# Optimization experiments

Measured on AMD Instinct MI355X. Metric: run time of the kernel, lower is better.

## Reference

```python
import jax, jax.numpy as jnp
import numpy as np

B, S, D = 32, 512, 768
M, T = 32, 30
H, DFF, L, E = 12, 3072, 4, 100000
HD = D // H


def _layer_norm(x, w, b):
    m = jnp.mean(x, axis=-1, keepdims=True)
    v = jnp.var(x, axis=-1, keepdims=True)
    return (x - m) * jax.lax.rsqrt(v + 1e-5) * w + b


def _encoder_layer(x, p):
    # torch.nn.TransformerEncoderLayer, batch_first, post-LN, relu, eval (no dropout)
    wi, bi, wo, bo, g1, b1, w1, c1, w2, c2, g2, b2 = p
    qkv = x @ wi.T + bi                                   # [B,M,3D]
    q, k, v = jnp.split(qkv, 3, axis=-1)
    q = q.reshape(B, M, H, HD)
    k = k.reshape(B, M, H, HD)
    v = v.reshape(B, M, H, HD)
    a = jnp.einsum('bqhd,bkhd->bhqk', q, k) / np.float32(np.sqrt(HD))
    a = jax.nn.softmax(a, axis=-1)
    o = jnp.einsum('bhqk,bkhd->bqhd', a, v).reshape(B, M, D)
    x = _layer_norm(x + o @ wo.T + bo, g1, b1)
    ff = jax.nn.relu(x @ w1.T + c1) @ w2.T + c2
    return _layer_norm(x + ff, g2, b2)


def _forward(lhs, attn_w, attn_b, Wi, Bi, Wo, Bo, G1, B1, W1, C1, W2, C2, G2, B2v,
             cls_w1, cls_w2, cls_b2, pos, emask):
    # Vectorized form of the source triple loop: token slot x of mention (i,j) is
    # copied from last_hidden_state[i, x] while no -1 has been seen (break) and
    # the mention is active (entity_attention_mask != 0).
    valid = jnp.cumprod((pos != -1).astype(jnp.int32), axis=-1) > 0      # [B,M,T]
    valid = valid & (emask[:, :, None] != 0)
    mentions = jnp.where(valid[..., None], lhs[:, None, :T, :], 0.0)     # [B,M,T,D]
    scores = jax.nn.softmax(jnp.einsum('bmtd,d->bmt', mentions, attn_w) + attn_b, axis=-1)
    x = jnp.einsum('bmt,bmtd->bmd', scores, mentions)                    # attention pool
    for l in range(L):
        x = _encoder_layer(x, (Wi[l], Bi[l], Wo[l], Bo[l], G1[l], B1[l],
                               W1[l], C1[l], W2[l], C2[l], G2[l], B2v[l]))
    return (x @ cls_w1.T) @ cls_w2.T + cls_b2                            # [B,M,E]


def setup_inputs() -> dict:
    key = jax.random.key(0)
    k = jax.random.split(key, 12)
    lhs = jax.random.normal(k[0], (B, S, D), jnp.float32)
    pos = jax.random.randint(k[1], (B, M, T), 0, S)
    lens = jax.random.randint(k[2], (B, M), 0, T + 1)
    pos = jnp.where(jnp.arange(T)[None, None, :] < lens[..., None], pos, -1)
    emask = jax.random.randint(k[3], (B, M), 0, 2)
    s = 0.02
    return {
        'last_hidden_state': lhs,
        'attn_w': jax.random.normal(k[4], (D,), jnp.float32) * s,
        'attn_b': jnp.zeros((), jnp.float32),
        'in_proj_w': jax.random.normal(k[5], (L, 3 * D, D), jnp.float32) * s,
        'in_proj_b': jnp.zeros((L, 3 * D), jnp.float32),
        'out_w': jax.random.normal(k[6], (L, D, D), jnp.float32) * s,
        'out_b': jnp.zeros((L, D), jnp.float32),
        'ln1_w': jnp.ones((L, D), jnp.float32),
        'ln1_b': jnp.zeros((L, D), jnp.float32),
        'lin1_w': jax.random.normal(k[7], (L, DFF, D), jnp.float32) * s,
        'lin1_b': jnp.zeros((L, DFF), jnp.float32),
        'lin2_w': jax.random.normal(k[8], (L, D, DFF), jnp.float32) * s,
        'lin2_b': jnp.zeros((L, D), jnp.float32),
        'ln2_w': jnp.ones((L, D), jnp.float32),
        'ln2_b': jnp.zeros((L, D), jnp.float32),
        'cls_w1': jax.random.normal(k[9], (100, D), jnp.float32) * s,
        'cls_w2': jax.random.normal(k[10], (E, 100), jnp.float32) * s,
        'cls_b2': jnp.zeros((E,), jnp.float32),
        'entity_position_ids': pos,
        'entity_attention_mask': emask,
    }


def reference(last_hidden_state, attn_w, attn_b, in_proj_w, in_proj_b, out_w, out_b,
              ln1_w, ln1_b, lin1_w, lin1_b, lin2_w, lin2_b, ln2_w, ln2_b,
              cls_w1, cls_w2, cls_b2, entity_position_ids, entity_attention_mask):
    return _forward(last_hidden_state, attn_w, attn_b, in_proj_w, in_proj_b, out_w, out_b,
                    ln1_w, ln1_b, lin1_w, lin1_b, lin2_w, lin2_b, ln2_w, ln2_b,
                    cls_w1, cls_w2, cls_b2, entity_position_ids, entity_attention_mask)
```

## Files before the change

### kernel.cpp

```cpp
#include <hip/hip_runtime.h>

constexpr int Bc = 32, Sc = 512, Dc = 768, Mc = 32, Tc = 30;
constexpr int Hc = 12, DFFc = 3072, Lc = 4, Ec = 100000, HDc = 64;
constexpr int TOK = Bc * Mc;
constexpr int KC2 = 128;

typedef float floatx4 __attribute__((ext_vector_type(4)));
typedef __bf16 bfrag8 __attribute__((ext_vector_type(8)));
typedef unsigned short usx8 __attribute__((ext_vector_type(8)));
typedef unsigned short usx4 __attribute__((ext_vector_type(4)));

__device__ __forceinline__ unsigned short f32_to_bf16(float f) {
    unsigned int u = __float_as_uint(f);
    unsigned int r = (u + 0x7FFFu + ((u >> 16) & 1u)) >> 16;
    return (unsigned short)r;
}

__device__ __forceinline__ void gload_lds16(const void* gsrc, void* lds) {
    __builtin_amdgcn_global_load_lds((const unsigned int*)gsrc, (unsigned int*)lds, 16, 0, 0);
}

struct CvtSegs {
    const float* src[7];
    unsigned short* dst[7];
    unsigned int end[7];
    unsigned int total;
};

constexpr int FB_CVT1 = 1536, FB_CVT2 = 512, FB_POOL = TOK;

__global__ __launch_bounds__(256)
void front_kernel(CvtSegs a, const float* __restrict__ cw2, unsigned short* __restrict__ bw_c2,
                  const float* __restrict__ lhs, const float* __restrict__ attn_w,
                  const int* __restrict__ pos, const int* __restrict__ emask,
                  float* __restrict__ x0, unsigned short* __restrict__ x0b) {
    const int bid = blockIdx.x;
    const int tid = threadIdx.x;

    if (bid < FB_CVT1) {
        const unsigned int stride = FB_CVT1 * 256;
        for (unsigned int i = bid * 256 + tid; i < a.total; i += stride) {
            int s = 0;
            while (i >= a.end[s]) ++s;
            const unsigned int off = i - (s ? a.end[s - 1] : 0u);
            usx4 o = (usx4)0;
            if (a.src[s]) {
                floatx4 v = *(const floatx4*)(a.src[s] + 4 * (size_t)off);
                #pragma unroll
                for (int j = 0; j < 4; ++j) o[j] = f32_to_bf16(v[j]);
            }
            *(usx4*)(a.dst[s] + 4 * (size_t)off) = o;
        }
        return;
    }
    if (bid < FB_CVT1 + FB_CVT2) {
        const int total = Ec * (KC2 / 8);
        const int stride = FB_CVT2 * 256;
        for (int c = (bid - FB_CVT1) * 256 + tid; c < total; c += stride) {
            const int row = c >> 4, j = c & 15;
            const int col0 = j * 8;
            const float* sp = cw2 + (size_t)row * 100 + col0;
            usx8 o = (usx8)0;
            if (col0 + 8 <= 100) {
                floatx4 v0 = *(const floatx4*)(sp);
                floatx4 v1 = *(const floatx4*)(sp + 4);
                #pragma unroll
                for (int jj = 0; jj < 4; ++jj) { o[jj] = f32_to_bf16(v0[jj]); o[4 + jj] = f32_to_bf16(v1[jj]); }
            } else if (col0 < 100) {
                #pragma unroll
                for (int jj = 0; jj < 8; ++jj)
                    if (col0 + jj < 100) o[jj] = f32_to_bf16(sp[jj]);
            }
            *(usx8*)(bw_c2 + (size_t)row * KC2 + col0) = o;
        }
        return;
    }

    const int bm = bid - (FB_CVT1 + FB_CVT2);
    const int b = bm >> 5;
    __shared__ float s_logit[32];
    __shared__ float s_w[32];
    __shared__ int s_valid[32];

    if (tid == 0) {
        int em = emask[bm];
        int ok = 1;
        for (int t = 0; t < Tc; ++t) {
            if (pos[bm * Tc + t] == -1) ok = 0;
            s_valid[t] = (ok && em) ? 1 : 0;
        }
    }
    __syncthreads();

    const int wid = tid >> 6, lane = tid & 63;
    for (int t = wid; t < Tc; t += 4) {
        float p = 0.f;
        const float* row = lhs + ((size_t)b * Sc + t) * Dc;
        for (int d = lane; d < Dc; d += 64) p += row[d] * attn_w[d];
        #pragma unroll
        for (int off = 32; off > 0; off >>= 1) p += __shfl_down(p, off);
        if (lane == 0) s_logit[t] = s_valid[t] ? p : 0.0f;
    }
    __syncthreads();
    if (tid == 0) {
        float mx = -1e30f;
        for (int t = 0; t < Tc; ++t) mx = fmaxf(mx, s_logit[t]);
        float sum = 0.f;
        for (int t = 0; t < Tc; ++t) { float e = expf(s_logit[t] - mx); s_w[t] = e; sum += e; }
        float inv = 1.0f / sum;
        for (int t = 0; t < Tc; ++t) s_w[t] = s_valid[t] ? s_w[t] * inv : 0.0f;
    }
    __syncthreads();
    for (int d = tid; d < Dc; d += 256) {
        float acc = 0.f;
        for (int t = 0; t < Tc; ++t) acc += s_w[t] * lhs[((size_t)b * Sc + t) * Dc + d];
        x0[(size_t)bm * Dc + d] = acc;
        x0b[(size_t)bm * Dc + d] = f32_to_bf16(acc);
    }
}

template <int BM, int BN, int WM, int WN, int OUTBF>
__global__ __launch_bounds__(256)
void gemm_bf16_kernel(const unsigned short* __restrict__ A, int lda,
                      const unsigned short* __restrict__ B, int ldb,
                      const float* __restrict__ bias, void* __restrict__ Cv,
                      int ldc, int M, int N, int K, int relu, int nxReal) {
    constexpr int BK = 64;
    __shared__ unsigned short lA[2][BM * BK];
    __shared__ unsigned short lB[2][BN * BK];

    int bx, by;
    if (nxReal > 0) {
        const int gx = gridDim.x, gy = gridDim.y;
        const int lb = blockIdx.y * gx + blockIdx.x;
        const int xcd = lb & 7, p = lb >> 3;
        const int pq = p / gy;
        bx = xcd * (gx >> 3) + pq;
        by = p - pq * gy;
        if (bx >= nxReal) return;
    } else {
        bx = blockIdx.x; by = blockIdx.y;
    }
    const int z = blockIdx.z;
    A += (size_t)z * K;
    B += (size_t)z * K;

    const int tid = threadIdx.x;
    const int bm0 = by * BM;
    const int bn0 = bx * BN;

    const int wid = tid >> 6;
    const int lane = tid & 63;
    const int quad = lane >> 4;
    const int l16 = lane & 15;
    const int wr = (wid >> 1) * (WM * 16);
    const int wc = (wid & 1) * (WN * 16);

    floatx4 acc[WM][WN] = {};

    auto stageA = [&](int buf, int k0) {
        #pragma unroll
        for (int it = 0; it < BM / 32; ++it) {
            const int chunk = wid * (BM / 32) + it;
            const int boff = chunk * 1024 + lane * 16;
            const int row = boff >> 7;
            const int cb = (boff & 127) ^ ((row & 7) << 4);
            gload_lds16((const char*)(A + (size_t)(bm0 + row) * lda + k0) + cb,
                        &lA[buf][chunk * 512]);
        }
    };
    auto stageB = [&](int buf, int k0) {
        #pragma unroll
        for (int it = 0; it < BN / 32; ++it) {
            const int chunk = wid * (BN / 32) + it;
            const int boff = chunk * 1024 + lane * 16;
            const int row = boff >> 7;
            const int cb = (boff & 127) ^ ((row & 7) << 4);
            gload_lds16((const char*)(B + (size_t)(bn0 + row) * ldb + k0) + cb,
                        &lB[buf][chunk * 512]);
        }
    };

    stageA(0, 0);
    stageB(0, 0);
    __syncthreads();

    int c = 0;
    for (int k0 = 0; k0 < K; k0 += BK, c ^= 1) {
        const int kn = k0 + BK;
        const bool more = (kn < K);
        if (more) { stageA(c ^ 1, kn); stageB(c ^ 1, kn); }
        const unsigned short* bA = lA[c];
        const unsigned short* bB = lB[c];
        #pragma unroll
        for (int kk = 0; kk < BK; kk += 32) {
            bfrag8 af[WM], bfr[WN];
            #pragma unroll
            for (int i = 0; i < WM; ++i) {
                const int rowA = wr + i * 16 + l16;
                af[i] = *(const bfrag8*)((const char*)bA + rowA * 128 +
                                         ((kk * 2 + quad * 16) ^ ((rowA & 7) << 4)));
            }
            #pragma unroll
            for (int j = 0; j < WN; ++j) {
                const int rowB = wc + j * 16 + l16;
                bfr[j] = *(const bfrag8*)((const char*)bB + rowB * 128 +
                                          ((kk * 2 + quad * 16) ^ ((rowB & 7) << 4)));
            }
            #pragma unroll
            for (int i = 0; i < WM; ++i)
                #pragma unroll
                for (int j = 0; j < WN; ++j)
                    acc[i][j] = __builtin_amdgcn_mfma_f32_16x16x32_bf16(af[i], bfr[j], acc[i][j], 0, 0, 0);
        }
        if (more) __syncthreads();
    }

    #pragma unroll
    for (int i = 0; i < WM; ++i) {
        #pragma unroll
        for (int j = 0; j < WN; ++j) {
            const int col = bn0 + wc + j * 16 + l16;
            if (col < N) {
                const int row0 = bm0 + wr + i * 16 + quad * 4;
                const float bv = bias ? bias[col] : 0.0f;
                #pragma unroll
                for (int r = 0; r < 4; ++r) {
                    float v = acc[i][j][r] + bv;
                    if (relu) v = fmaxf(v, 0.0f);
                    const size_t idx = (size_t)z * M * ldc + (size_t)(row0 + r) * ldc + col;
                    if (OUTBF) ((unsigned short*)Cv)[idx] = f32_to_bf16(v);
                    else       ((float*)Cv)[idx] = v;
                }
            }
        }
    }
}

__global__ __launch_bounds__(256)
void attn_kernel(const float* __restrict__ qkv, unsigned short* __restrict__ outb) {
    const int bh = blockIdx.x;
    const int b = bh / Hc, h = bh % Hc;
    const int tid = threadIdx.x;
    __shared__ float sQ[32][65];
    __shared__ float sK[32][65];
    __shared__ float sV[32][65];
    __shared__ float sS[32][33];

    const int m = tid >> 3;
    const int c0 = (tid & 7) * 8;
    {
        const size_t rbase = ((size_t)(b * 32 + m)) * (3 * Dc);
        #pragma unroll
        for (int j = 0; j < 8; ++j) {
            sQ[m][c0 + j] = qkv[rbase + h * HDc + c0 + j];
            sK[m][c0 + j] = qkv[rbase + Dc + h * HDc + c0 + j];
            sV[m][c0 + j] = qkv[rbase + 2 * Dc + h * HDc + c0 + j];
        }
    }
    __syncthreads();

    #pragma unroll
    for (int u = 0; u < 4; ++u) {
        const int e = tid * 4 + u;
        const int q = e >> 5, k = e & 31;
        float s = 0.f;
        #pragma unroll
        for (int d = 0; d < HDc; ++d) s += sQ[q][d] * sK[k][d];
        sS[q][k] = s * 0.125f;
    }
    __syncthreads();
    if (tid < 32) {
        float mx = -1e30f;
        for (int k = 0; k < 32; ++k) mx = fmaxf(mx, sS[tid][k]);
        float sum = 0.f;
        for (int k = 0; k < 32; ++k) { float e = expf(sS[tid][k] - mx); sS[tid][k] = e; sum += e; }
        const float inv = 1.0f / sum;
        for (int k = 0; k < 32; ++k) sS[tid][k] *= inv;
    }
    __syncthreads();
    float o[8] = {};
    for (int k = 0; k < 32; ++k) {
        const float p = sS[m][k];
        #pragma unroll
        for (int j = 0; j < 8; ++j) o[j] += p * sV[k][c0 + j];
    }
    usx8 o8;
    #pragma unroll
    for (int j = 0; j < 8; ++j) o8[j] = f32_to_bf16(o[j]);
    *(usx8*)(&outb[((size_t)(b * 32 + m)) * Dc + h * HDc + c0]) = o8;
}

__global__ __launch_bounds__(256)
void addln_kernel(const float* __restrict__ xa, const float* __restrict__ xs, int nslab,
                  const float* __restrict__ badd, const float* __restrict__ g,
                  const float* __restrict__ be, float* __restrict__ outf,
                  unsigned short* __restrict__ outb) {
    const int row = blockIdx.x;
    const int tid = threadIdx.x;
    __shared__ float red[8];
    float v[3];
    float s = 0.f, sq = 0.f;
    #pragma unroll
    for (int i = 0; i < 3; ++i) {
        const int d = tid + i * 256;
        float x = xa[(size_t)row * Dc + d] + badd[d];
        for (int sl = 0; sl < nslab; ++sl)
            x += xs[((size_t)sl * TOK + row) * Dc + d];
        v[i] = x; s += x; sq += x * x;
    }
    #pragma unroll
    for (int off = 32; off > 0; off >>= 1) {
        s += __shfl_down(s, off);
        sq += __shfl_down(sq, off);
    }
    if ((tid & 63) == 0) { red[tid >> 6] = s; red[4 + (tid >> 6)] = sq; }
    __syncthreads();
    const float ts = red[0] + red[1] + red[2] + red[3];
    const float tq = red[4] + red[5] + red[6] + red[7];
    const float mean = ts * (1.0f / Dc);
    const float var = tq * (1.0f / Dc) - mean * mean;
    const float inv = rsqrtf(var + 1e-5f);
    #pragma unroll
    for (int i = 0; i < 3; ++i) {
        const int d = tid + i * 256;
        const float y = (v[i] - mean) * inv * g[d] + be[d];
        outf[(size_t)row * Dc + d] = y;
        outb[(size_t)row * Dc + d] = f32_to_bf16(y);
    }
}

extern "C" void kernel_launch(void* const* d_in, const int* in_sizes, int n_in,
                              void* d_out, int out_size, void* d_ws, size_t ws_size,
                              hipStream_t stream) {
    const float* lhs   = (const float*)d_in[0];
    const float* attnw = (const float*)d_in[1];
    const float* ipw = (const float*)d_in[3];
    const float* ipb = (const float*)d_in[4];
    const float* oww = (const float*)d_in[5];
    const float* owb = (const float*)d_in[6];
    const float* g1  = (const float*)d_in[7];
    const float* b1  = (const float*)d_in[8];
    const float* l1w = (const float*)d_in[9];
    const float* l1b = (const float*)d_in[10];
    const float* l2w = (const float*)d_in[11];
    const float* l2b = (const float*)d_in[12];
    const float* g2  = (const float*)d_in[13];
    const float* b2  = (const float*)d_in[14];
    const float* cw1 = (const float*)d_in[15];
    const float* cw2 = (const float*)d_in[16];
    const float* cb2 = (const float*)d_in[17];
    const int* pos   = (const int*)d_in[18];
    const int* emask = (const int*)d_in[19];
    float* out = (float*)d_out;

    constexpr size_t N_IP = (size_t)Lc * 3 * Dc * Dc;
    constexpr size_t N_OW = (size_t)Lc * Dc * Dc;
    constexpr size_t N_L1 = (size_t)Lc * DFFc * Dc;
    constexpr size_t N_L2 = (size_t)Lc * Dc * DFFc;
    constexpr size_t N_C1 = (size_t)KC2 * Dc;

    char* ws = (char*)d_ws;
    unsigned short* bw_c2 = (unsigned short*)ws;
    unsigned short* bufCb = bw_c2 + (size_t)Ec * KC2;

    constexpr size_t F_XA   = (size_t)TOK * Dc;
    constexpr size_t F_QKV  = (size_t)TOK * 3 * Dc;
    constexpr size_t F_SLAB = (size_t)4 * TOK * Dc;
    constexpr size_t S_ACT  = (size_t)TOK * Dc;
    constexpr size_t S_FFH  = (size_t)TOK * DFFc;
    constexpr size_t tail_bytes =
        4 * (F_XA + F_XA + F_QKV + F_SLAB) +
        2 * (N_IP + N_OW + N_L1 + N_L2 + N_C1 + 3 * S_ACT + S_FFH);

    const size_t out_bytes = (size_t)out_size * 4;
    char* tail = (char*)d_out + ((out_bytes - tail_bytes) & ~(size_t)255);

    float* xA   = (float*)tail;
    float* xB   = xA + F_XA;
    float* qkvb = xB + F_XA;
    float* bufS = qkvb + F_QKV;
    unsigned short* bw_ip = (unsigned short*)(bufS + F_SLAB);
    unsigned short* bw_ow = bw_ip + N_IP;
    unsigned short* bw_l1 = bw_ow + N_OW;
    unsigned short* bw_l2 = bw_l1 + N_L1;
    unsigned short* bw_c1 = bw_l2 + N_L2;
    unsigned short* xAb   = bw_c1 + N_C1;
    unsigned short* xBb   = xAb + S_ACT;
    unsigned short* attnb = xBb + S_ACT;
    unsigned short* bufHb = attnb + S_ACT;

    {
        CvtSegs segs{};
        const float* srcs[6] = {ipw, oww, l1w, l2w, cw1, nullptr};
        unsigned short* dsts[6] = {bw_ip, bw_ow, bw_l1, bw_l2, bw_c1, bw_c1 + (size_t)100 * Dc};
        const unsigned int cnt[6] = {(unsigned)(N_IP / 4), (unsigned)(N_OW / 4),
                                     (unsigned)(N_L1 / 4), (unsigned)(N_L2 / 4),
                                     (unsigned)(100 * Dc / 4), (unsigned)(28 * Dc / 4)};
        unsigned int acc = 0;
        for (int i = 0; i < 6; ++i) { segs.src[i] = srcs[i]; segs.dst[i] = dsts[i]; acc += cnt[i]; segs.end[i] = acc; }
        segs.src[6] = nullptr; segs.dst[6] = dsts[5]; segs.end[6] = 0xFFFFFFFFu;
        segs.total = acc;
        front_kernel<<<FB_CVT1 + FB_CVT2 + FB_POOL, 256, 0, stream>>>(
            segs, cw2, bw_c2, lhs, attnw, pos, emask, xA, xAb);
    }

    auto g64 = [&](const unsigned short* A, int lda, const unsigned short* B, int ldb,
                   const float* bias, void* C, int ldc, int N, int K, int relu,
                   int ks, int outbf, bool swz) {
        int gx = (N + 63) / 64, nx = -1;
        if (swz) { nx = gx; gx = (gx + 7) & ~7; }
        dim3 grid(gx, TOK / 64, ks);
        if (outbf) gemm_bf16_kernel<64, 64, 2, 2, 1><<<grid, 256, 0, stream>>>(A, lda, B, ldb, bias, C, ldc, TOK, N, K, relu, nx);
        else       gemm_bf16_kernel<64, 64, 2, 2, 0><<<grid, 256, 0, stream>>>(A, lda, B, ldb, bias, C, ldc, TOK, N, K, relu, nx);
    };

    for (int l = 0; l < Lc; ++l) {
        g64(xAb, Dc, bw_ip + (size_t)l * 3 * Dc * Dc, Dc, ipb + (size_t)l * 3 * Dc,
            qkvb, 3 * Dc, 3 * Dc, Dc, 0, 1, 0, false);
        attn_kernel<<<Bc * Hc, 256, 0, stream>>>(qkvb, attnb);
        g64(attnb, Dc, bw_ow + (size_t)l * Dc * Dc, Dc, nullptr,
            bufS, Dc, Dc, Dc / 4, 0, 4, 0, false);
        addln_kernel<<<TOK, 256, 0, stream>>>(xA, bufS, 4, owb + (size_t)l * Dc,
                                              g1 + (size_t)l * Dc, b1 + (size_t)l * Dc, xB, xBb);
        g64(xBb, Dc, bw_l1 + (size_t)l * DFFc * Dc, Dc, l1b + (size_t)l * DFFc,
            bufHb, DFFc, DFFc, Dc, 1, 1, 1, true);
        g64(bufHb, DFFc, bw_l2 + (size_t)l * Dc * DFFc, DFFc, nullptr,
            bufS, Dc, Dc, DFFc / 4, 0, 4, 0, false);
        addln_kernel<<<TOK, 256, 0, stream>>>(xB, bufS, 4, l2b + (size_t)l * Dc,
                                              g2 + (size_t)l * Dc, b2 + (size_t)l * Dc, xA, xAb);
    }

    g64(xAb, Dc, bw_c1, Dc, nullptr, bufCb, KC2, KC2, Dc, 0, 1, 1, false);
    {
        int nx = (Ec + 127) / 128;
        int gx = (nx + 7) & ~7;
        dim3 grid(gx, TOK / 128, 1);
        gemm_bf16_kernel<128, 128, 4, 4, 0><<<grid, 256, 0, stream>>>(
            bufCb, KC2, bw_c2, KC2, cb2, out, Ec, TOK, Ec, KC2, 0, nx);
    }
}
```

Baseline: 1.023 ms.

## Fuse QKV projection into attention kernel and drop GEMM double buffering

Replaces the separate QKV GEMM and attention kernel with one kernel per (batch, head). Each block computes its 32x192 Q/K/V slice with MFMA, keeps it in shared memory, and runs softmax attention there, so the fp32 QKV buffer never goes to global memory and one launch per layer disappears. The generic GEMM also moves from double-buffered LDS staging to a single buffer with a sync before and after compute. That cuts LDS use and may raise occupancy, but load latency is no longer overlapped with MFMA work in every GEMM, including the large classifier GEMM.

```diff
diff --git a/kernel.cpp b/kernel.cpp
--- a/kernel.cpp
+++ b/kernel.cpp
@@ -126,8 +126,8 @@
                       const float* __restrict__ bias, void* __restrict__ Cv,
                       int ldc, int M, int N, int K, int relu, int nxReal) {
     constexpr int BK = 64;
-    __shared__ unsigned short lA[2][BM * BK];
-    __shared__ unsigned short lB[2][BN * BK];
+    __shared__ unsigned short lA[BM * BK];
+    __shared__ unsigned short lB[BN * BK];
 
     int bx, by;
     if (nxReal > 0) {
@@ -158,7 +158,7 @@
 
     floatx4 acc[WM][WN] = {};
 
-    auto stageA = [&](int buf, int k0) {
+    for (int k0 = 0; k0 < K; k0 += BK) {
         #pragma unroll
         for (int it = 0; it < BM / 32; ++it) {
             const int chunk = wid * (BM / 32) + it;
@@ -166,10 +166,8 @@
             const int row = boff >> 7;
             const int cb = (boff & 127) ^ ((row & 7) << 4);
             gload_lds16((const char*)(A + (size_t)(bm0 + row) * lda + k0) + cb,
-                        &lA[buf][chunk * 512]);
-        }
-    };
-    auto stageB = [&](int buf, int k0) {
+                        &lA[chunk * 512]);
+        }
         #pragma unroll
         for (int it = 0; it < BN / 32; ++it) {
             const int chunk = wid * (BN / 32) + it;
@@ -177,34 +175,22 @@
             const int row = boff >> 7;
             const int cb = (boff & 127) ^ ((row & 7) << 4);
             gload_lds16((const char*)(B + (size_t)(bn0 + row) * ldb + k0) + cb,
-                        &lB[buf][chunk * 512]);
-        }
-    };
-
-    stageA(0, 0);
-    stageB(0, 0);
-    __syncthreads();
-
-    int c = 0;
-    for (int k0 = 0; k0 < K; k0 += BK, c ^= 1) {
-        const int kn = k0 + BK;
-        const bool more = (kn < K);
-        if (more) { stageA(c ^ 1, kn); stageB(c ^ 1, kn); }
-        const unsigned short* bA = lA[c];
-        const unsigned short* bB = lB[c];
+                        &lB[chunk * 512]);
+        }
+        __syncthreads();
         #pragma unroll
         for (int kk = 0; kk < BK; kk += 32) {
             bfrag8 af[WM], bfr[WN];
             #pragma unroll
             for (int i = 0; i < WM; ++i) {
                 const int rowA = wr + i * 16 + l16;
-                af[i] = *(const bfrag8*)((const char*)bA + rowA * 128 +
+                af[i] = *(const bfrag8*)((const char*)lA + rowA * 128 +
                                          ((kk * 2 + quad * 16) ^ ((rowA & 7) << 4)));
             }
             #pragma unroll
             for (int j = 0; j < WN; ++j) {
                 const int rowB = wc + j * 16 + l16;
-                bfr[j] = *(const bfrag8*)((const char*)bB + rowB * 128 +
+                bfr[j] = *(const bfrag8*)((const char*)lB + rowB * 128 +
                                           ((kk * 2 + quad * 16) ^ ((rowB & 7) << 4)));
             }
             #pragma unroll
@@ -213,7 +199,7 @@
                 for (int j = 0; j < WN; ++j)
                     acc[i][j] = __builtin_amdgcn_mfma_f32_16x16x32_bf16(af[i], bfr[j], acc[i][j], 0, 0, 0);
         }
-        if (more) __syncthreads();
+        __syncthreads();
     }
 
     #pragma unroll
@@ -238,35 +224,94 @@
 }
 
 __global__ __launch_bounds__(256)
-void attn_kernel(const float* __restrict__ qkv, unsigned short* __restrict__ outb) {
+void fqa_kernel(const unsigned short* __restrict__ xAb,
+                const unsigned short* __restrict__ bw_ip_l,
+                const float* __restrict__ ipb_l,
+                unsigned short* __restrict__ attnb) {
+    __shared__ __align__(16) char smem[29696];
+    unsigned short* sA = (unsigned short*)smem;
+    unsigned short* sB = (unsigned short*)(smem + 4096);
+    float* qkvf = (float*)smem;
+    float (*sS)[33] = (float(*)[33])(smem + 25344);
+
     const int bh = blockIdx.x;
-    const int b = bh / Hc, h = bh % Hc;
+    const int b32 = (bh / Hc) * 32;
+    const int h = bh % Hc;
     const int tid = threadIdx.x;
-    __shared__ float sQ[32][65];
-    __shared__ float sK[32][65];
-    __shared__ float sV[32][65];
-    __shared__ float sS[32][33];
+    const int wid = tid >> 6, lane = tid & 63;
+    const int quad = lane >> 4, l16 = lane & 15;
+
+    floatx4 acc[2][3] = {};
+
+    for (int k0 = 0; k0 < Dc; k0 += 64) {
+        #pragma unroll
+        for (int it = 0; it < 7; ++it) {
+            const int c = wid * 7 + it;
+            if (c < 4) {
+                const int boff = c * 1024 + lane * 16;
+                const int row = boff >> 7;
+                const int cb = (boff & 127) ^ ((row & 7) << 4);
+                gload_lds16((const char*)(xAb + (size_t)(b32 + row) * Dc + k0) + cb,
+                            &sA[c * 512]);
+            } else {
+                const int boff = (c - 4) * 1024 + lane * 16;
+                const int row = boff >> 7;
+                const int cb = (boff & 127) ^ ((row & 7) << 4);
+                const int grow = (row >> 6) * Dc + h * 64 + (row & 63);
+                gload_lds16((const char*)(bw_ip_l + (size_t)grow * Dc + k0) + cb,
+                            &sB[(c - 4) * 512]);
+            }
+        }
+        __syncthreads();
+        #pragma unroll
+        for (int kk = 0; kk < 64; kk += 32) {
+            bfrag8 af[2], bfr[3];
+            #pragma unroll
+            for (int i = 0; i < 2; ++i) {
+                const int rowA = i * 16 + l16;
+                af[i] = *(const bfrag8*)((const char*)sA + rowA * 128 +
+                                         ((kk * 2 + quad * 16) ^ ((rowA & 7) << 4)));
+            }
+            #pragma unroll
+            for (int j = 0; j < 3; ++j) {
+                const int rowB = (wid * 3 + j) * 16 + l16;
+                bfr[j] = *(const bfrag8*)((const char*)sB + rowB * 128 +
+                                          ((kk * 2 + quad * 16) ^ ((rowB & 7) << 4)));
+            }
+            #pragma unroll
+            for (int i = 0; i < 2; ++i)
+                #pragma unroll
+                for (int j = 0; j < 3; ++j)
+                    acc[i][j] = __builtin_amdgcn_mfma_f32_16x16x32_bf16(af[i], bfr[j], acc[i][j], 0, 0, 0);
+        }
+        __syncthreads();
+    }
+
+    #pragma unroll
+    for (int i = 0; i < 2; ++i) {
+        #pragma unroll
+        for (int j = 0; j < 3; ++j) {
+            const int col = (wid * 3 + j) * 16 + l16;
+            const int p = col >> 6, pc = col & 63;
+            const float bv = ipb_l[p * Dc + h * 64 + pc];
+            const int row0 = i * 16 + quad * 4;
+            #pragma unroll
+            for (int r = 0; r < 4; ++r)
+                qkvf[(p * 32 + row0 + r) * 66 + pc] = acc[i][j][r] + bv;
+        }
+    }
+    __syncthreads();
 
     const int m = tid >> 3;
     const int c0 = (tid & 7) * 8;
-    {
-        const size_t rbase = ((size_t)(b * 32 + m)) * (3 * Dc);
-        #pragma unroll
-        for (int j = 0; j < 8; ++j) {
-            sQ[m][c0 + j] = qkv[rbase + h * HDc + c0 + j];
-            sK[m][c0 + j] = qkv[rbase + Dc + h * HDc + c0 + j];
-            sV[m][c0 + j] = qkv[rbase + 2 * Dc + h * HDc + c0 + j];
-        }
-    }
-    __syncthreads();
-
     #pragma unroll
     for (int u = 0; u < 4; ++u) {
         const int e = tid * 4 + u;
         const int q = e >> 5, k = e & 31;
         float s = 0.f;
         #pragma unroll
-        for (int d = 0; d < HDc; ++d) s += sQ[q][d] * sK[k][d];
+        for (int d = 0; d < HDc; ++d)
+            s += qkvf[q * 66 + d] * qkvf[(32 + k) * 66 + d];
         sS[q][k] = s * 0.125f;
     }
     __syncthreads();
@@ -283,12 +328,12 @@
     for (int k = 0; k < 32; ++k) {
         const float p = sS[m][k];
         #pragma unroll
-        for (int j = 0; j < 8; ++j) o[j] += p * sV[k][c0 + j];
+        for (int j = 0; j < 8; ++j) o[j] += p * qkvf[(64 + k) * 66 + c0 + j];
     }
     usx8 o8;
     #pragma unroll
     for (int j = 0; j < 8; ++j) o8[j] = f32_to_bf16(o[j]);
-    *(usx8*)(&outb[((size_t)(b * 32 + m)) * Dc + h * HDc + c0]) = o8;
+    *(usx8*)(&attnb[((size_t)(b32 + m)) * Dc + h * HDc + c0]) = o8;
 }
 
 __global__ __launch_bounds__(256)
@@ -416,9 +461,8 @@
     };
 
     for (int l = 0; l < Lc; ++l) {
-        g64(xAb, Dc, bw_ip + (size_t)l * 3 * Dc * Dc, Dc, ipb + (size_t)l * 3 * Dc,
-            qkvb, 3 * Dc, 3 * Dc, Dc, 0, 1, 0, false);
-        attn_kernel<<<Bc * Hc, 256, 0, stream>>>(qkvb, attnb);
+        fqa_kernel<<<Bc * Hc, 256, 0, stream>>>(
+            xAb, bw_ip + (size_t)l * 3 * Dc * Dc, ipb + (size_t)l * 3 * Dc, attnb);
         g64(attnb, Dc, bw_ow + (size_t)l * Dc * Dc, Dc, nullptr,
             bufS, Dc, Dc, Dc / 4, 0, 4, 0, false);
         addln_kernel<<<TOK, 256, 0, stream>>>(xA, bufS, 4, owb + (size_t)l * Dc,
```

Result: faster. 981.8 us (-4.0%).
